# Kernel tuning notes

Hardware: AMD Instinct MI355X
Metric: run time of the kernel (lower is better)

The kernel has to match this reference:

```python
import jax, jax.numpy as jnp
import numpy as np

D_MODEL = 1024
H = 16
T = 1024
B = 8

def setup_inputs() -> dict:
    key = jax.random.key(0)
    k0, k1, k2, k3, k4 = jax.random.split(key, 5)
    return {
        "x": jax.random.normal(k0, (B, T, D_MODEL), dtype=jnp.float32),
        "Wq": jax.random.normal(k1, (D_MODEL, D_MODEL), dtype=jnp.float32),
        "Wk": jax.random.normal(k2, (D_MODEL, D_MODEL), dtype=jnp.float32),
        "Wv": jax.random.normal(k3, (D_MODEL, D_MODEL), dtype=jnp.float32),
        "Wp": jax.random.normal(k4, (D_MODEL, D_MODEL), dtype=jnp.float32),
    }

def reference(x, Wq, Wk, Wv, Wp):
    b, t, d = x.shape
    dh = d // H
    # projections
    q = (x @ Wq).reshape(b, t, H, dh)
    k = (x @ Wk).reshape(b, t, H, dh)
    v = (x @ Wv).reshape(b, t, H, dh)
    # [b, h, t, t] attention scores, scaled by sqrt(d_head)
    scores = jnp.einsum("bqhd,bkhd->bhqk", q, k) / jnp.sqrt(jnp.float32(dh))
    attn = jax.nn.softmax(scores, axis=-1)
    # [b, h, t, dh] -> [b, t, d]
    out = jnp.einsum("bhqk,bkhd->bqhd", attn, v).reshape(b, t, d)
    return out @ Wp
```

## Files before the change

kernel.cpp:

```cpp
#include <hip/hip_runtime.h>
#include <math.h>


typedef unsigned short u16;
typedef unsigned int u32;
typedef __bf16  bf16x8 __attribute__((ext_vector_type(8)));
typedef unsigned short u16x8 __attribute__((ext_vector_type(8)));
typedef unsigned short u16x4 __attribute__((ext_vector_type(4)));
typedef short s16x4 __attribute__((ext_vector_type(4)));
typedef unsigned int u32x2 __attribute__((ext_vector_type(2)));
typedef float f32x4 __attribute__((ext_vector_type(4)));

#define MFMA16(a,b,c) __builtin_amdgcn_mfma_f32_16x16x32_bf16((a),(b),(c),0,0,0)
#define MFMA16K16(a,b,c) __builtin_amdgcn_mfma_f32_16x16x16bf16_1k((a),(b),(c),0,0,0)

static __device__ __forceinline__ u16 f2b(float f){
  unsigned u = __builtin_bit_cast(unsigned, f);
  u += 0x7fffu + ((u >> 16) & 1u);
  return (u16)(u >> 16);
}
static __device__ __forceinline__ float b2f(u16 h){
  unsigned u = ((unsigned)h) << 16;
  return __builtin_bit_cast(float, u);
}
static __device__ __forceinline__ bf16x8 ldsfrag(const u16* p){
  return __builtin_bit_cast(bf16x8, *(const u16x8*)p);
}
static __device__ __forceinline__ u32 packhi(float fa, float fb){
  return __builtin_amdgcn_perm(__builtin_bit_cast(u32, fa),
                               __builtin_bit_cast(u32, fb), 0x07060302u);
}
static __device__ __forceinline__ void gld16(const void* g, void* l){
  __builtin_amdgcn_global_load_lds(
      (const __attribute__((address_space(1))) void*)g,
      (__attribute__((address_space(3))) void*)l, 16, 0, 0);
}


__global__ __launch_bounds__(256) void split_x_kernel(
    const float* __restrict__ x, u16* __restrict__ xh, u16* __restrict__ xl, int n)
{
  int i = (blockIdx.x * 256 + threadIdx.x) * 8;
  if (i >= n) return;
  float4 v0 = *(const float4*)(x + i);
  float4 v1 = *(const float4*)(x + i + 4);
  float vv[8] = {v0.x, v0.y, v0.z, v0.w, v1.x, v1.y, v1.z, v1.w};
  u16x8 hv, lv;
#pragma unroll
  for (int j = 0; j < 8; j++){
    u16 hb = f2b(vv[j]);
    hv[j] = hb;
    lv[j] = f2b(vv[j] - b2f(hb));
  }
  *(u16x8*)(xh + i) = hv;
  *(u16x8*)(xl + i) = lv;
}

__global__ __launch_bounds__(256) void transpose4_kernel(
    const float* __restrict__ Wq, const float* __restrict__ Wk,
    const float* __restrict__ Wv, const float* __restrict__ Wp,
    u16* __restrict__ qh_, u16* __restrict__ ql_,
    u16* __restrict__ kh_, u16* __restrict__ kl_,
    u16* __restrict__ vt_, u16* __restrict__ pt_)
{
  __shared__ float t[32][33];
  const int z = blockIdx.z;
  const float* W = (z == 0) ? Wq : (z == 1) ? Wk : (z == 2) ? Wv : Wp;
  u16* Th = (z == 0) ? qh_ : (z == 1) ? kh_ : (z == 2) ? vt_ : pt_;
  u16* Tl = (z == 0) ? ql_ : (z == 1) ? kl_ : nullptr;
  int n0 = blockIdx.x * 32, k0 = blockIdx.y * 32;
  int tx = threadIdx.x, ty = threadIdx.y;
#pragma unroll
  for (int i = 0; i < 4; i++){
    int k = k0 + ty + i * 8;
    t[ty + i * 8][tx] = W[(size_t)k * 1024 + n0 + tx];
  }
  __syncthreads();
#pragma unroll
  for (int i = 0; i < 4; i++){
    int n = n0 + ty + i * 8;
    float v = t[tx][ty + i * 8];
    u16 h = f2b(v);
    Th[(size_t)n * 1024 + k0 + tx] = h;
    if (Tl) Tl[(size_t)n * 1024 + k0 + tx] = f2b(v - b2f(h));
  }
}

template<int OUTMODE>
__global__ __launch_bounds__(256) void gemm_bt_kernel(
    const u16* __restrict__ A, const u16* __restrict__ Bt, void* __restrict__ Cv,
    int M, int N, int K)
{
  __shared__ __attribute__((aligned(16))) u16 lA[4096], lB[4096];
  const int tid = threadIdx.x, lane = tid & 63, wave = tid >> 6;
  const int quad = lane >> 4, l15 = lane & 15;
  const int row0 = blockIdx.x * 128, col0 = blockIdx.y * 128;
  const int wm = wave >> 1, wn = wave & 1;
  const int sr = lane >> 2, sc = (lane & 3) * 8;
  f32x4 acc[4][4];
#pragma unroll
  for (int mt = 0; mt < 4; mt++)
#pragma unroll
    for (int nt = 0; nt < 4; nt++) acc[mt][nt] = (f32x4)0.0f;

  for (int k0 = 0; k0 < K; k0 += 32){
#pragma unroll
    for (int i = 0; i < 2; i++){
      int c = wave * 2 + i;
      gld16(A  + (size_t)(row0 + c * 16 + sr) * K + k0 + sc, &lA[c * 512]);
      gld16(Bt + (size_t)(col0 + c * 16 + sr) * K + k0 + sc, &lB[c * 512]);
    }
    __syncthreads();
    bf16x8 a[4], b[4];
#pragma unroll
    for (int t = 0; t < 4; t++){
      a[t] = ldsfrag(&lA[(wm * 64 + t * 16 + l15) * 32 + quad * 8]);
      b[t] = ldsfrag(&lB[(wn * 64 + t * 16 + l15) * 32 + quad * 8]);
    }
#pragma unroll
    for (int mt = 0; mt < 4; mt++)
#pragma unroll
      for (int nt = 0; nt < 4; nt++)
        acc[mt][nt] = MFMA16(a[mt], b[nt], acc[mt][nt]);
    __syncthreads();
  }
  if (OUTMODE == 2){
#pragma unroll
    for (int mt = 0; mt < 4; mt++)
#pragma unroll
      for (int nt = 0; nt < 4; nt++){
        int row = row0 + wm * 64 + mt * 16 + quad * 4;
        int col = col0 + wn * 64 + nt * 16 + l15;
        int bb = row >> 10, tt = row & 1023;
        int hh = (col >> 6) & 15, d = col & 63;
        int bhI = bb * 16 + hh;
        int ktile = tt >> 7, fkt = (tt >> 4) & 7, qF = (tt >> 2) & 3;
        int nd = d >> 4, l15F = d & 15;
        size_t idx = ((((size_t)(bhI * 8 + ktile) * 8 + fkt) * 4 + nd) * 64
                      + qF * 16 + l15F) * 4;
        u16x4 vals;
#pragma unroll
        for (int r = 0; r < 4; r++) vals[r] = f2b(acc[mt][nt][r]);
        *(u16x4*)(((u16*)Cv) + idx) = vals;
      }
  } else {
#pragma unroll
    for (int mt = 0; mt < 4; mt++)
#pragma unroll
      for (int nt = 0; nt < 4; nt++)
#pragma unroll
        for (int r = 0; r < 4; r++){
          int row = row0 + wm * 64 + mt * 16 + quad * 4 + r;
          int col = col0 + wn * 64 + nt * 16 + l15;
          ((float*)Cv)[(size_t)row * N + col] = acc[mt][nt][r];
        }
  }
}

__global__ __launch_bounds__(256) void gemm_qk_kernel(
    const u16* __restrict__ Ah, const u16* __restrict__ Al,
    const u16* __restrict__ Bh, const u16* __restrict__ Bl,
    u16* __restrict__ Qhf, u16* __restrict__ Qlf,
    u16* __restrict__ Khf, u16* __restrict__ Klf, int M, int N, int K)
{
  __shared__ __attribute__((aligned(16))) u16 lAh[4096], lAl[4096], lBh[4096], lBl[4096];
  const int tid = threadIdx.x, lane = tid & 63, wave = tid >> 6;
  const int quad = lane >> 4, l15 = lane & 15;
  const int row0 = blockIdx.x * 128, col0 = blockIdx.y * 128;
  const int wm = wave >> 1, wn = wave & 1;
  const int sr = lane >> 2, sc = (lane & 3) * 8;
  f32x4 acc[4][4];
#pragma unroll
  for (int mt = 0; mt < 4; mt++)
#pragma unroll
    for (int nt = 0; nt < 4; nt++) acc[mt][nt] = (f32x4)0.0f;

  for (int k0 = 0; k0 < K; k0 += 32){
#pragma unroll
    for (int i = 0; i < 2; i++){
      int c = wave * 2 + i;
      size_t ao = (size_t)(row0 + c * 16 + sr) * K + k0 + sc;
      size_t bo = (size_t)(col0 + c * 16 + sr) * K + k0 + sc;
      gld16(Ah + ao, &lAh[c * 512]);
      gld16(Al + ao, &lAl[c * 512]);
      gld16(Bh + bo, &lBh[c * 512]);
      gld16(Bl + bo, &lBl[c * 512]);
    }
    __syncthreads();
    bf16x8 ah[4], al[4], bh[4], bl[4];
#pragma unroll
    for (int t = 0; t < 4; t++){
      int aoff = (wm * 64 + t * 16 + l15) * 32 + quad * 8;
      int boff = (wn * 64 + t * 16 + l15) * 32 + quad * 8;
      ah[t] = ldsfrag(&lAh[aoff]);  al[t] = ldsfrag(&lAl[aoff]);
      bh[t] = ldsfrag(&lBh[boff]);  bl[t] = ldsfrag(&lBl[boff]);
    }
#pragma unroll
    for (int mt = 0; mt < 4; mt++)
#pragma unroll
      for (int nt = 0; nt < 4; nt++){
        acc[mt][nt] = MFMA16(al[mt], bh[nt], acc[mt][nt]);
        acc[mt][nt] = MFMA16(ah[mt], bl[nt], acc[mt][nt]);
        acc[mt][nt] = MFMA16(ah[mt], bh[nt], acc[mt][nt]);
      }
    __syncthreads();
  }
  const bool isQ = (col0 < 1024);
#pragma unroll
  for (int mt = 0; mt < 4; mt++)
#pragma unroll
    for (int nt = 0; nt < 4; nt++)
#pragma unroll
      for (int r = 0; r < 4; r++){
        int row = row0 + wm * 64 + mt * 16 + quad * 4 + r;
        int col = col0 + wn * 64 + nt * 16 + l15;
        int bb = row >> 10, tt = row & 1023;
        int hh = (col >> 6) & 15, d = col & 63;
        int bhI = bb * 16 + hh;
        int kc = d >> 5, qF = (d >> 3) & 3, j = d & 7;
        float v = acc[mt][nt][r];
        u16 hi = f2b(v);
        u16 lo = f2b(v - b2f(hi));
        if (isQ){
          int qtile = tt >> 7, rr = tt & 127;
          int wv = rr >> 5, mtF = (rr >> 4) & 1, l15F = tt & 15;
          size_t idx = ((((size_t)(bhI * 8 + qtile) * 4 + wv) * 2 + mtF) * 2 + kc) * 512
                       + (qF * 16 + l15F) * 8 + j;
          Qhf[idx] = hi; Qlf[idx] = lo;
        } else {
          int ktile = tt >> 7, fkt = (tt >> 4) & 7, l15F = tt & 15;
          size_t idx = (((size_t)(bhI * 8 + ktile) * 8 + fkt) * 2 + kc) * 512
                       + (qF * 16 + l15F) * 8 + j;
          Khf[idx] = hi; Klf[idx] = lo;
        }
      }
}

__global__ __launch_bounds__(256, 3) void attn_kernel(
    const u16* __restrict__ Qhf, const u16* __restrict__ Qlf,
    const u16* __restrict__ Khf, const u16* __restrict__ Klf,
    const u16* __restrict__ Vf, u16* __restrict__ O)
{
  __shared__ __attribute__((aligned(16))) u16 lKh[2][4096], lKl[2][4096], lV[2][4096];
  const int tid = threadIdx.x, lane = tid & 63, wave = tid >> 6;
  const int quad = lane >> 4, l15 = lane & 15;
  const int qt = blockIdx.x >> 7, bh = blockIdx.x & 127;
  const int b = bh >> 4, h = bh & 15;
  const int q0 = qt * 128;
  const float BETA = 0.18033688011112042f;

  bf16x8 qh[2][2], ql[2][2];
  {
    size_t qbase = (size_t)(bh * 8 + qt) * 8192 + wave * 2048 + lane * 8;
    u16* sh = &lKh[0][0];  u16* sl = &lKl[0][0];
#pragma unroll
    for (int i = 0; i < 4; i++){
      gld16(Qhf + qbase + i * 512, sh + wave * 2048 + i * 512);
      gld16(Qlf + qbase + i * 512, sl + wave * 2048 + i * 512);
    }
    __syncthreads();
#pragma unroll
    for (int mt = 0; mt < 2; mt++)
#pragma unroll
      for (int kc = 0; kc < 2; kc++){
        int off = wave * 2048 + (mt * 2 + kc) * 512 + lane * 8;
        qh[mt][kc] = ldsfrag(sh + off);
        ql[mt][kc] = ldsfrag(sl + off);
      }
    __syncthreads();
  }

  float m_i[2] = {-3.0e38f, -3.0e38f}, l_i[2] = {0.0f, 0.0f};
  f32x4 o_acc[2][4];
#pragma unroll
  for (int mt = 0; mt < 2; mt++)
#pragma unroll
    for (int nd = 0; nd < 4; nd++) o_acc[mt][nd] = (f32x4)0.0f;

  const size_t pan = (size_t)bh * 65536;
#pragma unroll
  for (int i = 0; i < 2; i++){
    int c = wave * 2 + i;
    gld16(Khf + pan + c * 512 + lane * 8, &lKh[0][c * 512]);
    gld16(Klf + pan + c * 512 + lane * 8, &lKl[0][c * 512]);
    gld16(Vf  + pan + c * 512 + lane * 8, &lV [0][c * 512]);
  }

#pragma unroll 1
  for (int j = 0; j < 16; j++){
    const int cur = j & 1;
    __syncthreads();
    if (j < 15){
      size_t nb = pan + (size_t)(j + 1) * 4096;
      const int nxt = cur ^ 1;
#pragma unroll
      for (int i = 0; i < 2; i++){
        int c = wave * 2 + i;
        gld16(Khf + nb + c * 512 + lane * 8, &lKh[nxt][c * 512]);
        gld16(Klf + nb + c * 512 + lane * 8, &lKl[nxt][c * 512]);
        gld16(Vf  + nb + c * 512 + lane * 8, &lV [nxt][c * 512]);
      }
    }

    f32x4 s[2][4];
#pragma unroll
    for (int qt2 = 0; qt2 < 2; qt2++)
#pragma unroll
      for (int f4 = 0; f4 < 4; f4++) s[qt2][f4] = (f32x4)0.0f;
#pragma unroll
    for (int f4 = 0; f4 < 4; f4++){
      int aoff = f4 * 1024 + lane * 8;
      bf16x8 kh0 = ldsfrag(&lKh[cur][aoff]);
      bf16x8 kh1 = ldsfrag(&lKh[cur][aoff + 512]);
      bf16x8 kl0 = ldsfrag(&lKl[cur][aoff]);
      bf16x8 kl1 = ldsfrag(&lKl[cur][aoff + 512]);
#pragma unroll
      for (int qt2 = 0; qt2 < 2; qt2++){
        s[qt2][f4] = MFMA16(kl0, qh[qt2][0], s[qt2][f4]);
        s[qt2][f4] = MFMA16(kl1, qh[qt2][1], s[qt2][f4]);
        s[qt2][f4] = MFMA16(kh0, ql[qt2][0], s[qt2][f4]);
        s[qt2][f4] = MFMA16(kh1, ql[qt2][1], s[qt2][f4]);
        s[qt2][f4] = MFMA16(kh0, qh[qt2][0], s[qt2][f4]);
        s[qt2][f4] = MFMA16(kh1, qh[qt2][1], s[qt2][f4]);
      }
    }

    float alpha[2];
#pragma unroll
    for (int qt2 = 0; qt2 < 2; qt2++){
      f32x4 mv = s[qt2][0];
#pragma unroll
      for (int f4 = 1; f4 < 4; f4++){
        mv[0] = fmaxf(mv[0], s[qt2][f4][0]); mv[1] = fmaxf(mv[1], s[qt2][f4][1]);
        mv[2] = fmaxf(mv[2], s[qt2][f4][2]); mv[3] = fmaxf(mv[3], s[qt2][f4][3]);
      }
      float mx = fmaxf(fmaxf(mv[0], mv[1]), fmaxf(mv[2], mv[3]));
      mx = fmaxf(mx, __shfl_xor(mx, 16));
      mx = fmaxf(mx, __shfl_xor(mx, 32));
      float mn = fmaxf(m_i[qt2], mx);
      alpha[qt2] = __builtin_amdgcn_exp2f((m_i[qt2] - mn) * BETA);
      m_i[qt2] = mn;
      float mb = mn * BETA;
      f32x4 ps = (f32x4)0.0f;
#pragma unroll
      for (int f4 = 0; f4 < 4; f4++)
#pragma unroll
        for (int r = 0; r < 4; r++){
          float p = __builtin_amdgcn_exp2f(s[qt2][f4][r] * BETA - mb);
          s[qt2][f4][r] = p;
          ps[r] += p;
        }
      float rs = (ps[0] + ps[1]) + (ps[2] + ps[3]);
      rs += __shfl_xor(rs, 16);
      rs += __shfl_xor(rs, 32);
      l_i[qt2] = l_i[qt2] * alpha[qt2] + rs;
    }

#pragma unroll
    for (int mt = 0; mt < 2; mt++)
#pragma unroll
      for (int r = 0; r < 4; r++){
        float ar = __shfl(alpha[mt], quad * 4 + r);
#pragma unroll
        for (int nd = 0; nd < 4; nd++) o_acc[mt][nd][r] *= ar;
      }

#pragma unroll
    for (int f4 = 0; f4 < 4; f4++){
      s16x4 vb[4];
#pragma unroll
      for (int nd = 0; nd < 4; nd++)
        vb[nd] = __builtin_bit_cast(s16x4,
                   *(const u16x4*)&lV[cur][(f4 * 4 + nd) * 256 + lane * 4]);
#pragma unroll
      for (int qt2 = 0; qt2 < 2; qt2++){
        u32x2 pd;
        pd[0] = packhi(s[qt2][f4][1], s[qt2][f4][0]);
        pd[1] = packhi(s[qt2][f4][3], s[qt2][f4][2]);
        s16x4 pa = __builtin_bit_cast(s16x4, pd);
#pragma unroll
        for (int nd = 0; nd < 4; nd++)
          o_acc[qt2][nd] = MFMA16K16(pa, vb[nd], o_acc[qt2][nd]);
      }
    }
  }

#pragma unroll
  for (int mt = 0; mt < 2; mt++)
#pragma unroll
    for (int r = 0; r < 4; r++){
      float lr = __shfl(l_i[mt], quad * 4 + r);
      float inv = 1.0f / lr;
      int t = q0 + wave * 32 + mt * 16 + quad * 4 + r;
      size_t rowoff = (size_t)(b * 1024 + t) * 1024 + h * 64;
#pragma unroll
      for (int nd = 0; nd < 4; nd++)
        O[rowoff + nd * 16 + l15] = f2b(o_acc[mt][nd][r] * inv);
    }
}

extern "C" void kernel_launch(void* const* d_in, const int* in_sizes, int n_in,
                              void* d_out, int out_size, void* d_ws, size_t ws_size,
                              hipStream_t stream)
{
  const float* x  = (const float*)d_in[0];
  const float* Wq = (const float*)d_in[1];
  const float* Wk = (const float*)d_in[2];
  const float* Wv = (const float*)d_in[3];
  const float* Wp = (const float*)d_in[4];
  float* out = (float*)d_out;
  char* ws = (char*)d_ws;
  const size_t MB = 1024 * 1024;
  u16* xh   = (u16*)(ws + 0);
  u16* xl   = (u16*)(ws + 16 * MB);
  u16* wqkh = (u16*)(ws + 32 * MB);
  u16* wqkl = (u16*)(ws + 36 * MB);
  u16* wvt  = (u16*)(ws + 40 * MB);
  u16* wpt  = (u16*)(ws + 42 * MB);
  u16* Qhf  = (u16*)(ws + 44 * MB);
  u16* Qlf  = (u16*)(ws + 60 * MB);
  u16* Khf  = (u16*)(ws + 76 * MB);
  u16* Klf  = (u16*)(ws + 92 * MB);
  u16* Vf   = (u16*)(ws + 108 * MB);
  u16* obuf = xh;
  (void)in_sizes; (void)n_in; (void)out_size; (void)ws_size;

  split_x_kernel<<<4096, 256, 0, stream>>>(x, xh, xl, 8 * 1024 * 1024);
  transpose4_kernel<<<dim3(32, 32, 4), dim3(32, 8), 0, stream>>>(
      Wq, Wk, Wv, Wp, wqkh, wqkl, wqkh + 1024 * 1024, wqkl + 1024 * 1024, wvt, wpt);
  gemm_qk_kernel<<<dim3(64, 16), 256, 0, stream>>>(xh, xl, wqkh, wqkl,
                                                   Qhf, Qlf, Khf, Klf, 8192, 2048, 1024);
  gemm_bt_kernel<2><<<dim3(64, 8), 256, 0, stream>>>(xh, wvt, (void*)Vf, 8192, 1024, 1024);
  attn_kernel<<<1024, 256, 0, stream>>>(Qhf, Qlf, Khf, Klf, Vf, obuf);
  gemm_bt_kernel<0><<<dim3(64, 8), 256, 0, stream>>>(obuf, wpt, (void*)out, 8192, 1024, 1024);
}
```

Baseline: 355.2 us.

## Load Q/K/V fragments directly from global memory, dropping LDS staging in attention

The attention kernel no longer stages K, K-low and V tiles through double-buffered shared memory. Each wave now reads its MFMA fragments straight from global memory (relying on cache), which removes the LDS traffic and the block-wide barriers. The V output layout of the projection GEMM is rearranged so each lane can fetch 16-byte chunks holding two 4-element fragments. The trade-off is that K and V are re-read from L2 by all four waves with no explicit prefetch, which may expose global-memory latency.

```diff
diff --git a/kernel.cpp b/kernel.cpp
--- a/kernel.cpp
+++ b/kernel.cpp
@@ -23,6 +23,9 @@
   unsigned u = ((unsigned)h) << 16;
   return __builtin_bit_cast(float, u);
 }
+static __device__ __forceinline__ bf16x8 gfrag(const u16* p){
+  return __builtin_bit_cast(bf16x8, *(const u16x8*)p);
+}
 static __device__ __forceinline__ bf16x8 ldsfrag(const u16* p){
   return __builtin_bit_cast(bf16x8, *(const u16x8*)p);
 }
@@ -135,9 +138,10 @@
         int hh = (col >> 6) & 15, d = col & 63;
         int bhI = bb * 16 + hh;
         int ktile = tt >> 7, fkt = (tt >> 4) & 7, qF = (tt >> 2) & 3;
+        int j64 = ktile * 2 + (fkt >> 2), f4 = fkt & 3;
         int nd = d >> 4, l15F = d & 15;
-        size_t idx = ((((size_t)(bhI * 8 + ktile) * 8 + fkt) * 4 + nd) * 64
-                      + qF * 16 + l15F) * 4;
+        size_t idx = ((((size_t)(bhI * 16 + j64) * 4 + f4) * 2 + (nd >> 1)) * 512)
+                     + (qF * 16 + l15F) * 8 + (nd & 1) * 4;
         u16x4 vals;
 #pragma unroll
         for (int r = 0; r < 4; r++) vals[r] = f2b(acc[mt][nt][r]);
@@ -241,7 +245,6 @@
     const u16* __restrict__ Khf, const u16* __restrict__ Klf,
     const u16* __restrict__ Vf, u16* __restrict__ O)
 {
-  __shared__ __attribute__((aligned(16))) u16 lKh[2][4096], lKl[2][4096], lV[2][4096];
   const int tid = threadIdx.x, lane = tid & 63, wave = tid >> 6;
   const int quad = lane >> 4, l15 = lane & 15;
   const int qt = blockIdx.x >> 7, bh = blockIdx.x & 127;
@@ -251,23 +254,14 @@
 
   bf16x8 qh[2][2], ql[2][2];
   {
-    size_t qbase = (size_t)(bh * 8 + qt) * 8192 + wave * 2048 + lane * 8;
-    u16* sh = &lKh[0][0];  u16* sl = &lKl[0][0];
-#pragma unroll
-    for (int i = 0; i < 4; i++){
-      gld16(Qhf + qbase + i * 512, sh + wave * 2048 + i * 512);
-      gld16(Qlf + qbase + i * 512, sl + wave * 2048 + i * 512);
-    }
-    __syncthreads();
+    size_t qbase = ((size_t)(bh * 8 + qt) * 4 + wave) * 2048 + lane * 8;
 #pragma unroll
     for (int mt = 0; mt < 2; mt++)
 #pragma unroll
       for (int kc = 0; kc < 2; kc++){
-        int off = wave * 2048 + (mt * 2 + kc) * 512 + lane * 8;
-        qh[mt][kc] = ldsfrag(sh + off);
-        ql[mt][kc] = ldsfrag(sl + off);
-      }
-    __syncthreads();
+        qh[mt][kc] = gfrag(Qhf + qbase + (mt * 2 + kc) * 512);
+        ql[mt][kc] = gfrag(Qlf + qbase + (mt * 2 + kc) * 512);
+      }
   }
 
   float m_i[2] = {-3.0e38f, -3.0e38f}, l_i[2] = {0.0f, 0.0f};
@@ -277,51 +271,37 @@
 #pragma unroll
     for (int nd = 0; nd < 4; nd++) o_acc[mt][nd] = (f32x4)0.0f;
 
-  const size_t pan = (size_t)bh * 65536;
-#pragma unroll
-  for (int i = 0; i < 2; i++){
-    int c = wave * 2 + i;
-    gld16(Khf + pan + c * 512 + lane * 8, &lKh[0][c * 512]);
-    gld16(Klf + pan + c * 512 + lane * 8, &lKl[0][c * 512]);
-    gld16(Vf  + pan + c * 512 + lane * 8, &lV [0][c * 512]);
-  }
+  const size_t pan = (size_t)bh * 65536 + lane * 8;
 
 #pragma unroll 1
   for (int j = 0; j < 16; j++){
-    const int cur = j & 1;
-    __syncthreads();
-    if (j < 15){
-      size_t nb = pan + (size_t)(j + 1) * 4096;
-      const int nxt = cur ^ 1;
-#pragma unroll
-      for (int i = 0; i < 2; i++){
-        int c = wave * 2 + i;
-        gld16(Khf + nb + c * 512 + lane * 8, &lKh[nxt][c * 512]);
-        gld16(Klf + nb + c * 512 + lane * 8, &lKl[nxt][c * 512]);
-        gld16(Vf  + nb + c * 512 + lane * 8, &lV [nxt][c * 512]);
-      }
-    }
+    const u16* kb = Khf + pan + j * 4096;
+    const u16* lb = Klf + pan + j * 4096;
+    const u16* vb8 = Vf + pan + j * 4096;
 
     f32x4 s[2][4];
 #pragma unroll
     for (int qt2 = 0; qt2 < 2; qt2++)
 #pragma unroll
       for (int f4 = 0; f4 < 4; f4++) s[qt2][f4] = (f32x4)0.0f;
-#pragma unroll
-    for (int f4 = 0; f4 < 4; f4++){
-      int aoff = f4 * 1024 + lane * 8;
-      bf16x8 kh0 = ldsfrag(&lKh[cur][aoff]);
-      bf16x8 kh1 = ldsfrag(&lKh[cur][aoff + 512]);
-      bf16x8 kl0 = ldsfrag(&lKl[cur][aoff]);
-      bf16x8 kl1 = ldsfrag(&lKl[cur][aoff + 512]);
-#pragma unroll
-      for (int qt2 = 0; qt2 < 2; qt2++){
-        s[qt2][f4] = MFMA16(kl0, qh[qt2][0], s[qt2][f4]);
-        s[qt2][f4] = MFMA16(kl1, qh[qt2][1], s[qt2][f4]);
-        s[qt2][f4] = MFMA16(kh0, ql[qt2][0], s[qt2][f4]);
-        s[qt2][f4] = MFMA16(kh1, ql[qt2][1], s[qt2][f4]);
-        s[qt2][f4] = MFMA16(kh0, qh[qt2][0], s[qt2][f4]);
-        s[qt2][f4] = MFMA16(kh1, qh[qt2][1], s[qt2][f4]);
+#pragma unroll 1
+    for (int f4h = 0; f4h < 2; f4h++){
+#pragma unroll
+      for (int f4i = 0; f4i < 2; f4i++){
+        int f4 = f4h * 2 + f4i;
+        bf16x8 kh0 = gfrag(kb + f4 * 1024);
+        bf16x8 kh1 = gfrag(kb + f4 * 1024 + 512);
+        bf16x8 kl0 = gfrag(lb + f4 * 1024);
+        bf16x8 kl1 = gfrag(lb + f4 * 1024 + 512);
+#pragma unroll
+        for (int qt2 = 0; qt2 < 2; qt2++){
+          s[qt2][f4] = MFMA16(kl0, qh[qt2][0], s[qt2][f4]);
+          s[qt2][f4] = MFMA16(kl1, qh[qt2][1], s[qt2][f4]);
+          s[qt2][f4] = MFMA16(kh0, ql[qt2][0], s[qt2][f4]);
+          s[qt2][f4] = MFMA16(kh1, ql[qt2][1], s[qt2][f4]);
+          s[qt2][f4] = MFMA16(kh0, qh[qt2][0], s[qt2][f4]);
+          s[qt2][f4] = MFMA16(kh1, qh[qt2][1], s[qt2][f4]);
+        }
       }
     }
 
@@ -367,11 +347,14 @@
 
 #pragma unroll
     for (int f4 = 0; f4 < 4; f4++){
+      u16x8 v01 = *(const u16x8*)(vb8 + f4 * 1024);
+      u16x8 v23 = *(const u16x8*)(vb8 + f4 * 1024 + 512);
       s16x4 vb[4];
 #pragma unroll
-      for (int nd = 0; nd < 4; nd++)
-        vb[nd] = __builtin_bit_cast(s16x4,
-                   *(const u16x4*)&lV[cur][(f4 * 4 + nd) * 256 + lane * 4]);
+      for (int e = 0; e < 4; e++){
+        vb[0][e] = (short)v01[e];  vb[1][e] = (short)v01[e + 4];
+        vb[2][e] = (short)v23[e];  vb[3][e] = (short)v23[e + 4];
+      }
 #pragma unroll
       for (int qt2 = 0; qt2 < 2; qt2++){
         u32x2 pd;
```

Result: slower. 363.8 us (+2.4%).
